# Optimization experiments

Hardware: AMD Instinct MI355X
Metric: run time of the kernel (lower is better)

## Reference

```python
import jax, jax.numpy as jnp
import numpy as np
import math

H = 5120        # hidden_size
NH = 32         # num heads
HD = H // NH    # head_dim = 160
B = 1
S = 2048
TRAIN_SEQLEN = 8192
BASE = 10000.0


def _rotary_cos_sin(seq_len):
    # Eval-mode RotaryEmbedding: seq_len clamped to training_seqlen, NTK alpha + mscale (logN) scaling.
    eff = max(seq_len, TRAIN_SEQLEN)
    scale = eff / TRAIN_SEQLEN
    mscale = 1.0 if scale <= 1.0 else 0.1 * math.log(scale) + 1.0
    ntk_alpha = max(2 ** math.ceil(math.log(eff / 4096, 2) + 1) - 1, 1)
    base = BASE * ntk_alpha ** (HD / (HD - 2))
    inv_freq = 1.0 / base ** (np.arange(0, HD, 2, dtype=np.float64) / HD)
    t = np.arange(eff, dtype=np.float64)
    freqs = np.outer(t, inv_freq)              # [eff, HD/2]
    emb = np.concatenate([freqs, freqs], axis=-1)  # [eff, HD]
    cos = (mscale * np.cos(emb))[:seq_len].astype(np.float32)
    sin = (mscale * np.sin(emb))[:seq_len].astype(np.float32)
    return jnp.asarray(cos), jnp.asarray(sin)


def _rotate_half(x):
    x1, x2 = x[..., : HD // 2], x[..., HD // 2 :]
    return jnp.concatenate([-x2, x1], axis=-1)


def setup_inputs() -> dict:
    key = jax.random.key(0)
    ks = jax.random.split(key, 6)
    hidden_states = jax.random.normal(ks[0], (B, S, H), jnp.float32)
    residual = jax.random.normal(ks[1], (B, S, H), jnp.float32)
    # boolean causal mask, True = masked (matches masked_fill semantics)
    attention_mask = jnp.triu(jnp.ones((S, S), dtype=bool), k=1)[None, None]
    Wq = jax.random.normal(ks[2], (H, H), jnp.float32) * 0.02      # query: Linear(h, h, bias=False)
    Wkv = jax.random.normal(ks[3], (2 * H, H), jnp.float32) * 0.02  # key_value: Linear(h, 2h, bias=False)
    Wd = jax.random.normal(ks[4], (H, H), jnp.float32) * 0.02       # dense: Linear(h, h) with bias
    bd = jnp.zeros((H,), jnp.float32)
    return {
        "hidden_states": hidden_states,
        "residual": residual,
        "attention_mask": attention_mask,
        "Wq": Wq,
        "Wkv": Wkv,
        "Wd": Wd,
        "bd": bd,
    }


def reference(hidden_states, residual, attention_mask, Wq, Wkv, Wd, bd):
    b, s, h = hidden_states.shape
    # QKV projections (torch Linear: y = x @ W.T)
    q = jnp.einsum('bsh,oh->bso', hidden_states, Wq).reshape(b, s, NH, HD)
    kv = jnp.einsum('bsh,oh->bso', hidden_states, Wkv).reshape(b, s, NH, 2 * HD)
    k, v = kv[..., :HD], kv[..., HD:]
    # rotary embedding with logN mscale folded into cos/sin
    cos, sin = _rotary_cos_sin(s)               # [s, HD]
    cos = cos[None, :, None, :]
    sin = sin[None, :, None, :]
    q = q * cos + _rotate_half(q) * sin
    k = k * cos + _rotate_half(k) * sin
    inv_norm = 1.0 / math.sqrt(HD)
    scores = jnp.einsum('bqnd,bknd->bnqk', q, k) * inv_norm   # [b, nh, s, s]
    scores = jnp.where(attention_mask, jnp.finfo(scores.dtype).min, scores)
    probs = jax.nn.softmax(scores, axis=-1)
    # attention_dropout p=0.0 -> identity
    ctx = jnp.einsum('bnqk,bknd->bqnd', probs, v).reshape(b, s, h)
    out = ctx @ Wd.T + bd
    # dropout_add with hidden_dropout=0.0 (eval) -> residual + out
    return residual + out
```

## Files before the change

kernel.cpp:

```cpp
#include <hip/hip_runtime.h>
#include <cmath>

typedef unsigned short u16;
typedef unsigned int   u32;

using bf16x8 = __attribute__((ext_vector_type(8))) short;
using f32x4  = __attribute__((ext_vector_type(4))) float;

#define S_LEN 2048
#define NHEAD 32
#define HDIM  160
#define HID   5120
#define NQKV  15360

__device__ __forceinline__ f32x4 mfma16(bf16x8 a, bf16x8 b, f32x4 c) {
  return __builtin_amdgcn_mfma_f32_16x16x32_bf16(a, b, c, 0, 0, 0);
}

__device__ __forceinline__ u16 f2bf(float f) {
  u32 u = __builtin_bit_cast(u32, f);
  u += 0x7FFFu + ((u >> 16) & 1u);
  return (u16)(u >> 16);
}
__device__ __forceinline__ float bf2f(u16 h) {
  u32 u = ((u32)h) << 16;
  return __builtin_bit_cast(float, u);
}

__device__ __forceinline__ void gload16(const void* g, void* l) {
  __builtin_amdgcn_global_load_lds((const __attribute__((address_space(1))) void*)g,
                                   (__attribute__((address_space(3))) void*)l, 16, 0, 0);
}

__global__ void cvt_bf16_kernel(const float* __restrict__ in, u16* __restrict__ out, int n8) {
  int i = blockIdx.x * 256 + threadIdx.x;
  if (i >= n8) return;
  const float4* p = (const float4*)in + (size_t)i * 2;
  float4 a = p[0], b = p[1];
  uint4 o;
  o.x = (u32)f2bf(a.x) | ((u32)f2bf(a.y) << 16);
  o.y = (u32)f2bf(a.z) | ((u32)f2bf(a.w) << 16);
  o.z = (u32)f2bf(b.x) | ((u32)f2bf(b.y) << 16);
  o.w = (u32)f2bf(b.z) | ((u32)f2bf(b.w) << 16);
  ((uint4*)out)[i] = o;
}

__global__ void rope_table_kernel(float2* __restrict__ tab) {
  __shared__ double invf_s[80];
  int tid = threadIdx.x;
  if (tid < 80) {
    double base = 10000.0 * pow(3.0, 160.0 / 158.0);
    invf_s[tid] = pow(base, -((double)(2 * tid)) / 160.0);
  }
  __syncthreads();
  for (int i = blockIdx.x * 256 + tid; i < S_LEN * 80; i += gridDim.x * 256) {
    int s = i / 80, j = i % 80;
    double ang = fmod((double)s * invf_s[j], 6.283185307179586476925287);
    float a = (float)ang;
    tab[i] = make_float2(cosf(a), sinf(a));
  }
}

__global__ void rope_apply_kernel(const u16* __restrict__ src, const float2* __restrict__ tab,
                                  u16* __restrict__ dst, int headStride, int rowStride) {
  int i = blockIdx.x * 256 + threadIdx.x;
  if (i >= S_LEN * NHEAD * 80) return;
  int dp = i % 80; int sh = i / 80; int h = sh % NHEAD; int s = sh / NHEAD;
  int d = 2 * dp;
  const u16* row = src + (size_t)s * rowStride + h * headStride;
  u32 q01 = *(const u32*)&row[d];
  u32 p01 = *(const u32*)&row[d < 80 ? d + 80 : d - 80];
  int j = (d < 80) ? d : d - 80;
  float2 cs0 = tab[s * 80 + j];
  float2 cs1 = tab[s * 80 + j + 1];
  float q0 = bf2f((u16)(q01 & 0xffff)), q1 = bf2f((u16)(q01 >> 16));
  float p0 = bf2f((u16)(p01 & 0xffff)), p1 = bf2f((u16)(p01 >> 16));
  float sgn = (d < 80) ? -1.f : 1.f;
  float o0 = q0 * cs0.x + sgn * p0 * cs0.y;
  float o1 = q1 * cs1.x + sgn * p1 * cs1.y;
  u32 o = (u32)f2bf(o0) | ((u32)f2bf(o1) << 16);
  *(u32*)&dst[((size_t)h * S_LEN + s) * HDIM + d] = o;
}

__global__ void vtrans_kernel(const u16* __restrict__ src, u16* __restrict__ Vt, int rowStride) {
  __shared__ u16 T[HDIM][72];
  int h = blockIdx.y; int s0 = blockIdx.x * 64; int tid = threadIdx.x;
  for (int i = tid; i < 64 * 80; i += 256) {
    int s = i / 80, dp = i % 80;
    u32 v = *(const u32*)&src[(size_t)(s0 + s) * rowStride + h * 320 + 2 * dp];
    T[2 * dp][s]     = (u16)(v & 0xffff);
    T[2 * dp + 1][s] = (u16)(v >> 16);
  }
  __syncthreads();
  for (int i = tid; i < HDIM * 32; i += 256) {
    int d = i / 32, sp = i % 32;
    u32 v = (u32)T[d][2 * sp] | ((u32)T[d][2 * sp + 1] << 16);
    *(u32*)&Vt[((size_t)h * HDIM + d) * S_LEN + s0 + 2 * sp] = v;
  }
}

template<int EPI>
__global__ __launch_bounds__(512, 2) void gemm256(
    const u16* __restrict__ A, const u16* __restrict__ Bm, void* __restrict__ Cout,
    int M, int N, int K, const float* __restrict__ bias, const float* __restrict__ resid)
{
  __shared__ u16 As[2][2][8192];
  __shared__ u16 Bs[2][2][8192];
  int tid = threadIdx.x;
  int w = tid >> 6, l = tid & 63, l15 = l & 15, l4 = l >> 4;
  int wr = w >> 2, wc = w & 3;

  int nbx = gridDim.x;
  int nwg = nbx * gridDim.y;
  int lin = blockIdx.y * nbx + blockIdx.x;
  int cpx = nwg >> 3;
  int swz = (lin & 7) * cpx + (lin >> 3);
  int bm = (swz / nbx) * 256, bn = (swz % nbx) * 256;

  int srow = tid >> 2;
  int scol = ((tid & 3) * 8) ^ ((srow & 8) ? 16 : 0);
  const u16* gA0 = A  + (size_t)(bm +       srow) * K + scol;
  const u16* gA1 = A  + (size_t)(bm + 128 + srow) * K + scol;
  const u16* gB0 = Bm + (size_t)(bn +       srow) * K + scol;
  const u16* gB1 = Bm + (size_t)(bn + 128 + srow) * K + scol;
  int dstoff = w * 512;

  f32x4 acc[8][4];
#pragma unroll
  for (int i = 0; i < 8; i++)
#pragma unroll
    for (int j = 0; j < 4; j++) acc[i][j] = f32x4{0.f, 0.f, 0.f, 0.f};

  int cA = (l4 * 8) ^ ((l15 & 8) ? 16 : 0);
  const int NT = K >> 6;

  auto STAGE = [&](int kt, int p) {
    int k0 = kt << 6;
    gload16(gA0 + k0,      &As[p][0][dstoff]);
    gload16(gA0 + k0 + 32, &As[p][0][4096 + dstoff]);
    gload16(gA1 + k0,      &As[p][1][dstoff]);
    gload16(gA1 + k0 + 32, &As[p][1][4096 + dstoff]);
    gload16(gB0 + k0,      &Bs[p][0][dstoff]);
    gload16(gB0 + k0 + 32, &Bs[p][0][4096 + dstoff]);
    gload16(gB1 + k0,      &Bs[p][1][dstoff]);
    gload16(gB1 + k0 + 32, &Bs[p][1][4096 + dstoff]);
  };

  STAGE(0, 0);
  for (int kt = 0; kt < NT; ++kt) {
    int p = kt & 1;
    if (kt + 1 < NT) {
      STAGE(kt + 1, p ^ 1);
      asm volatile("s_waitcnt vmcnt(8)" ::: "memory");
    } else {
      asm volatile("s_waitcnt vmcnt(0)" ::: "memory");
    }
    __builtin_amdgcn_s_barrier();

    const u16* Ah = &As[p][wr][0];
    const u16* Bh = &Bs[p][wc >> 1][0];
    int bcol = (wc & 1) * 64;
#pragma unroll
    for (int kk = 0; kk < 2; ++kk) {
      bf16x8 aF[8], bF[4];
#pragma unroll
      for (int mi = 0; mi < 8; ++mi)
        aF[mi] = *(const bf16x8*)&Ah[kk * 4096 + (mi * 16 + l15) * 32 + cA];
#pragma unroll
      for (int ni = 0; ni < 4; ++ni)
        bF[ni] = *(const bf16x8*)&Bh[kk * 4096 + (bcol + ni * 16 + l15) * 32 + cA];
      __builtin_amdgcn_s_setprio(1);
#pragma unroll
      for (int mi = 0; mi < 8; ++mi)
#pragma unroll
        for (int ni = 0; ni < 4; ++ni)
          acc[mi][ni] = mfma16(aF[mi], bF[ni], acc[mi][ni]);
      __builtin_amdgcn_s_setprio(0);
    }
    __builtin_amdgcn_s_barrier();
  }

#pragma unroll
  for (int mi = 0; mi < 8; ++mi)
#pragma unroll
    for (int ni = 0; ni < 4; ++ni) {
      int row0 = bm + wr * 128 + mi * 16 + l4 * 4;
      int col  = bn + wc * 64 + ni * 16 + l15;
      if (EPI == 0) {
        u16* C = (u16*)Cout;
#pragma unroll
        for (int r = 0; r < 4; r++) C[(size_t)(row0 + r) * N + col] = f2bf(acc[mi][ni][r]);
      } else {
        float* C = (float*)Cout;
        float b = bias[col];
#pragma unroll
        for (int r = 0; r < 4; r++) {
          size_t idx = (size_t)(row0 + r) * N + col;
          C[idx] = acc[mi][ni][r] + b + resid[idx];
        }
      }
    }
}

template<int EPI>
__global__ __launch_bounds__(256, 2) void gemm_bt(
    const u16* __restrict__ A, const u16* __restrict__ Bm, void* __restrict__ Cout,
    int M, int N, int K, const float* __restrict__ bias, const float* __restrict__ resid)
{
  int tid = threadIdx.x;
  int wv = tid >> 6, l = tid & 63, l15 = l & 15, l4 = l >> 4;
  int nbx = gridDim.x;
  int nwg = nbx * gridDim.y;
  int lin = blockIdx.y * nbx + blockIdx.x;
  int cpx = nwg >> 3;
  int swz = (lin & 7) * cpx + (lin >> 3);
  int bm = (swz / nbx) * 128, bn = (swz % nbx) * 128;

  __shared__ u16 As[128 * 32], Bs[128 * 32];
  f32x4 acc[4][4];
#pragma unroll
  for (int i = 0; i < 4; i++)
#pragma unroll
    for (int j = 0; j < 4; j++) acc[i][j] = f32x4{0.f, 0.f, 0.f, 0.f};

  int wm = (wv >> 1) * 64, wn = (wv & 1) * 64;
  const u16* gA = A + (size_t)(bm + (tid >> 2)) * K + (tid & 3) * 8;
  const u16* gB = Bm + (size_t)(bn + (tid >> 2)) * K + (tid & 3) * 8;
  u16* ldsA = As + wv * 16 * 32;
  u16* ldsB = Bs + wv * 16 * 32;

  for (int k0 = 0; k0 < K; k0 += 32) {
    __syncthreads();
    gload16(gA + k0, ldsA);
    gload16(gA + (size_t)64 * K + k0, ldsA + 64 * 32);
    gload16(gB + k0, ldsB);
    gload16(gB + (size_t)64 * K + k0, ldsB + 64 * 32);
    __syncthreads();
    bf16x8 af[4], bfr[4];
#pragma unroll
    for (int i = 0; i < 4; i++) af[i] = *(const bf16x8*)&As[(wm + i * 16 + l15) * 32 + l4 * 8];
#pragma unroll
    for (int i = 0; i < 4; i++) bfr[i] = *(const bf16x8*)&Bs[(wn + i * 16 + l15) * 32 + l4 * 8];
#pragma unroll
    for (int mi = 0; mi < 4; mi++)
#pragma unroll
      for (int ni = 0; ni < 4; ni++) acc[mi][ni] = mfma16(af[mi], bfr[ni], acc[mi][ni]);
  }

#pragma unroll
  for (int mi = 0; mi < 4; mi++)
#pragma unroll
    for (int ni = 0; ni < 4; ni++) {
      int row0 = bm + wm + mi * 16 + l4 * 4;
      int col  = bn + wn + ni * 16 + l15;
      if (EPI == 0) {
        u16* C = (u16*)Cout;
#pragma unroll
        for (int r = 0; r < 4; r++) C[(size_t)(row0 + r) * N + col] = f2bf(acc[mi][ni][r]);
      } else {
        float* C = (float*)Cout;
        float b = bias[col];
#pragma unroll
        for (int r = 0; r < 4; r++) {
          size_t idx = (size_t)(row0 + r) * N + col;
          C[idx] = acc[mi][ni][r] + b + resid[idx];
        }
      }
    }
}

__global__ __launch_bounds__(512, 4) void attn_kernel(
    const u16* __restrict__ Qr, const u16* __restrict__ Kr,
    const u16* __restrict__ Vt, u16* __restrict__ ctx)
{
  int lin = blockIdx.x;
  int h  = lin & 31;
  int qx = (lin < 256) ? (15 - (lin >> 5)) : ((lin - 256) >> 5);
  int q0 = qx * 128;
  int tid = threadIdx.x;
  int w = tid >> 6, l = tid & 63, l15 = l & 15, l4 = l >> 4;
  int qb = q0 + w * 16;

  __shared__ u16 Ks[64][164];
  __shared__ u16 Vs[160][68];
  __shared__ u16 Plds[8][16][68];

  const u16* Qh = Qr + (size_t)h * S_LEN * HDIM;
  const u16* Kh = Kr + (size_t)h * S_LEN * HDIM;
  const u16* Vh = Vt + (size_t)h * HDIM * S_LEN;

  bf16x8 aQ[5];
#pragma unroll
  for (int kc = 0; kc < 5; kc++)
    aQ[kc] = *(const bf16x8*)&Qh[(size_t)(qb + l15) * HDIM + kc * 32 + l4 * 8];

  f32x4 accO[10];
#pragma unroll
  for (int dt = 0; dt < 10; dt++) accO[dt] = f32x4{0.f, 0.f, 0.f, 0.f};
  float mrun[4], lrun[4];
#pragma unroll
  for (int r = 0; r < 4; r++) { mrun[r] = -1e30f; lrun[r] = 0.f; }

  const float c2 = 0.07905694150420949f * 1.44269504088896f;
  int Tend = 2 * qx + 2;

  {
    uint4 rg[5];
#pragma unroll
    for (int i = 0; i < 5; i++) {
      int u = tid + 512 * i;
      if (u < 1280) { int row = u / 20, c = u % 20;
        rg[i] = *(const uint4*)&Kh[(size_t)row * HDIM + c * 8]; }
      else { int v = u - 1280; int row = v >> 3, c = v & 7;
        rg[i] = *(const uint4*)&Vh[(size_t)row * S_LEN + c * 8]; }
    }
#pragma unroll
    for (int i = 0; i < 5; i++) {
      int u = tid + 512 * i;
      if (u < 1280) { int row = u / 20, c = u % 20; *(uint4*)&Ks[row][c * 8] = rg[i]; }
      else { int v = u - 1280; int row = v >> 3, c = v & 7; *(uint4*)&Vs[row][c * 8] = rg[i]; }
    }
  }
  __syncthreads();

  for (int t = 0; t < Tend; ++t) {
    int k0 = t * 64;
    bool more = (t + 1 < Tend);
    uint4 rg[5];
    if (more) {
      int k1 = k0 + 64;
#pragma unroll
      for (int i = 0; i < 5; i++) {
        int u = tid + 512 * i;
        if (u < 1280) { int row = u / 20, c = u % 20;
          rg[i] = *(const uint4*)&Kh[(size_t)(k1 + row) * HDIM + c * 8]; }
        else { int v = u - 1280; int row = v >> 3, c = v & 7;
          rg[i] = *(const uint4*)&Vh[(size_t)row * S_LEN + k1 + c * 8]; }
      }
    }

    if (k0 <= qb + 15) {
      f32x4 s_[4];
#pragma unroll
      for (int nt = 0; nt < 4; nt++) s_[nt] = f32x4{0.f, 0.f, 0.f, 0.f};

#pragma unroll
      for (int kc = 0; kc < 5; kc++) {
        bf16x8 bK[4];
#pragma unroll
        for (int nt = 0; nt < 4; nt++)
          bK[nt] = *(const bf16x8*)&Ks[nt * 16 + l15][kc * 32 + l4 * 8];
        __builtin_amdgcn_s_setprio(1);
#pragma unroll
        for (int nt = 0; nt < 4; nt++) s_[nt] = mfma16(aQ[kc], bK[nt], s_[nt]);
        __builtin_amdgcn_s_setprio(0);
      }

      if (k0 + 63 > qb) {
#pragma unroll
        for (int nt = 0; nt < 4; nt++)
#pragma unroll
          for (int r = 0; r < 4; r++) {
            int kk = k0 + nt * 16 + l15;
            int qq = qb + l4 * 4 + r;
            if (kk > qq) s_[nt][r] = -1e30f;
          }
      }

      float sf[4];
#pragma unroll
      for (int r = 0; r < 4; r++) {
        float v = fmaxf(fmaxf(s_[0][r], s_[1][r]), fmaxf(s_[2][r], s_[3][r]));
#pragma unroll
        for (int m = 1; m <= 8; m <<= 1) v = fmaxf(v, __shfl_xor(v, m));
        float mnew = fmaxf(mrun[r], v);
        sf[r] = exp2f((mrun[r] - mnew) * c2);
        mrun[r] = mnew;
      }
      float rsum[4] = {0.f, 0.f, 0.f, 0.f};
#pragma unroll
      for (int nt = 0; nt < 4; nt++)
#pragma unroll
        for (int r = 0; r < 4; r++) {
          float p = exp2f((s_[nt][r] - mrun[r]) * c2);
          s_[nt][r] = p;
          rsum[r] += p;
        }
#pragma unroll
      for (int r = 0; r < 4; r++) {
        float v = rsum[r];
#pragma unroll
        for (int m = 1; m <= 8; m <<= 1) v += __shfl_xor(v, m);
        lrun[r] = lrun[r] * sf[r] + v;
      }
#pragma unroll
      for (int dt = 0; dt < 10; dt++)
#pragma unroll
        for (int r = 0; r < 4; r++) accO[dt][r] *= sf[r];
#pragma unroll
      for (int nt = 0; nt < 4; nt++)
#pragma unroll
        for (int r = 0; r < 4; r++)
          Plds[w][l4 * 4 + r][nt * 16 + l15] = f2bf(s_[nt][r]);

#pragma unroll
      for (int kc = 0; kc < 2; kc++) {
        bf16x8 aP = *(const bf16x8*)&Plds[w][l15][kc * 32 + l4 * 8];
        bf16x8 bV[10];
#pragma unroll
        for (int dt = 0; dt < 10; dt++)
          bV[dt] = *(const bf16x8*)&Vs[dt * 16 + l15][kc * 32 + l4 * 8];
        __builtin_amdgcn_s_setprio(1);
#pragma unroll
        for (int dt = 0; dt < 10; dt++)
          accO[dt] = mfma16(aP, bV[dt], accO[dt]);
        __builtin_amdgcn_s_setprio(0);
      }
    }

    __builtin_amdgcn_s_barrier();
    if (more) {
#pragma unroll
      for (int i = 0; i < 5; i++) {
        int u = tid + 512 * i;
        if (u < 1280) { int row = u / 20, c = u % 20; *(uint4*)&Ks[row][c * 8] = rg[i]; }
        else { int v = u - 1280; int row = v >> 3, c = v & 7; *(uint4*)&Vs[row][c * 8] = rg[i]; }
      }
      asm volatile("s_waitcnt lgkmcnt(0)" ::: "memory");
    }
    __builtin_amdgcn_s_barrier();
  }

  float inv[4];
#pragma unroll
  for (int r = 0; r < 4; r++) inv[r] = 1.0f / lrun[r];
#pragma unroll
  for (int dt = 0; dt < 10; dt++)
#pragma unroll
    for (int r = 0; r < 4; r++) {
      int q = qb + l4 * 4 + r;
      ctx[(size_t)q * HID + h * HDIM + dt * 16 + l15] = f2bf(accO[dt][r] * inv[r]);
    }
}

extern "C" void kernel_launch(void* const* d_in, const int* in_sizes, int n_in,
                              void* d_out, int out_size, void* d_ws, size_t ws_size,
                              hipStream_t stream) {
  const float* hs    = (const float*)d_in[0];
  const float* resid = (const float*)d_in[1];
  const float* Wq  = (const float*)d_in[3];
  const float* Wkv = (const float*)d_in[4];
  const float* Wd  = (const float*)d_in[5];
  const float* bd  = (const float*)d_in[6];
  float* out = (float*)d_out;

  char* ws = (char*)d_ws;
  const size_t SH = (size_t)S_LEN * HID;
  u16* Xb     = (u16*)(ws);                        size_t off = SH * 2;
  u16* Wqkvb  = (u16*)(ws + off);                  off += (size_t)3 * HID * HID * 2;
  u16* Wdb    = (u16*)(ws + off);                  off += (size_t)HID * HID * 2;
  u16* QKVraw = (u16*)(ws + off);                  off += (size_t)S_LEN * NQKV * 2;
  u16* Qr     = (u16*)(ws + off);                  off += SH * 2;
  u16* Kr     = (u16*)(ws + off);                  off += SH * 2;
  u16* Vt     = (u16*)(ws + off);                  off += SH * 2;
  u16* ctx    = (u16*)(ws + off);                  off += SH * 2;
  float2* tab = (float2*)(ws + off);               off += (size_t)S_LEN * 80 * 8;

  cvt_bf16_kernel<<<(int)(SH / 8 / 256), 256, 0, stream>>>(hs, Xb, (int)(SH / 8));
  cvt_bf16_kernel<<<HID * HID / 8 / 256, 256, 0, stream>>>(Wq, Wqkvb, HID * HID / 8);
  cvt_bf16_kernel<<<2 * HID * HID / 8 / 256, 256, 0, stream>>>(Wkv, Wqkvb + (size_t)HID * HID, 2 * HID * HID / 8);
  cvt_bf16_kernel<<<HID * HID / 8 / 256, 256, 0, stream>>>(Wd, Wdb, HID * HID / 8);

  rope_table_kernel<<<64, 256, 0, stream>>>(tab);

  gemm256<0><<<dim3(NQKV / 256, S_LEN / 256), 512, 0, stream>>>(
      Xb, Wqkvb, QKVraw, S_LEN, NQKV, HID, nullptr, nullptr);

  rope_apply_kernel<<<S_LEN * NHEAD * 80 / 256, 256, 0, stream>>>(QKVraw, tab, Qr, HDIM, NQKV);
  rope_apply_kernel<<<S_LEN * NHEAD * 80 / 256, 256, 0, stream>>>(QKVraw + HID, tab, Kr, 2 * HDIM, NQKV);
  vtrans_kernel<<<dim3(S_LEN / 64, NHEAD), 256, 0, stream>>>(QKVraw + HID + HDIM, Vt, NQKV);

  attn_kernel<<<512, 512, 0, stream>>>(Qr, Kr, Vt, ctx);

  gemm_bt<1><<<dim3(HID / 128, S_LEN / 128), 256, 0, stream>>>(
      ctx, Wdb, out, S_LEN, HID, HID, bd, resid);
}
```

Baseline: 1.008 ms.

## Split GEMM k-loop into four phases with staggered A/B prefetch

Restructures the bf16 MFMA GEMM main loop into four sub-phases, each covering one k-half and one half of the M rows. Each phase issues one slice of the global-to-LDS prefetch for later tiles (A or B, one k-half), so loads spread across the iteration instead of arriving in one burst. The LDS buffers are reorganised by k-half, and loads run up to two tiles ahead with adjusted vmcnt waits. Register pressure for A fragments drops from 8 to 4 per phase. The cost is many more workgroup barriers per iteration and more complex wait accounting, which could stall the waves.

```diff
diff --git a/kernel.cpp b/kernel.cpp
--- a/kernel.cpp
+++ b/kernel.cpp
@@ -119,11 +119,9 @@
 
   int srow = tid >> 2;
   int scol = ((tid & 3) * 8) ^ ((srow & 8) ? 16 : 0);
-  const u16* gA0 = A  + (size_t)(bm +       srow) * K + scol;
-  const u16* gA1 = A  + (size_t)(bm + 128 + srow) * K + scol;
-  const u16* gB0 = Bm + (size_t)(bn +       srow) * K + scol;
-  const u16* gB1 = Bm + (size_t)(bn + 128 + srow) * K + scol;
-  int dstoff = w * 512;
+  const u16* gAr = A  + (size_t)(bm + srow) * K + scol;
+  const u16* gBr = Bm + (size_t)(bn + srow) * K + scol;
+  int w512 = w * 512;
 
   f32x4 acc[8][4];
 #pragma unroll
@@ -133,50 +131,87 @@
 
   int cA = (l4 * 8) ^ ((l15 & 8) ? 16 : 0);
   const int NT = K >> 6;
-
-  auto STAGE = [&](int kt, int p) {
-    int k0 = kt << 6;
-    gload16(gA0 + k0,      &As[p][0][dstoff]);
-    gload16(gA0 + k0 + 32, &As[p][0][4096 + dstoff]);
-    gload16(gA1 + k0,      &As[p][1][dstoff]);
-    gload16(gA1 + k0 + 32, &As[p][1][4096 + dstoff]);
-    gload16(gB0 + k0,      &Bs[p][0][dstoff]);
-    gload16(gB0 + k0 + 32, &Bs[p][0][4096 + dstoff]);
-    gload16(gB1 + k0,      &Bs[p][1][dstoff]);
-    gload16(gB1 + k0 + 32, &Bs[p][1][4096 + dstoff]);
-  };
-
-  STAGE(0, 0);
+  int arow = wr * 128;
+  int brow = (wc >> 1) * 128 + (wc & 1) * 64;
+
+  auto STA = [&](int kt, int kk) { int p = kt & 1, ko = (kt << 6) + (kk << 5);
+    gload16(gAr + ko, &As[p][kk][w512]);
+    gload16(gAr + (size_t)128 * K + ko, &As[p][kk][4096 + w512]); };
+  auto STB = [&](int kt, int kk) { int p = kt & 1, ko = (kt << 6) + (kk << 5);
+    gload16(gBr + ko, &Bs[p][kk][w512]);
+    gload16(gBr + (size_t)128 * K + ko, &Bs[p][kk][4096 + w512]); };
+
+  STB(0, 0); STA(0, 0); STB(0, 1); STA(0, 1);
+  if (NT > 1) { STB(1, 0); STA(1, 0); STB(1, 1); }
+  asm volatile("s_waitcnt vmcnt(6)" ::: "memory");
+  __builtin_amdgcn_s_barrier();
+
   for (int kt = 0; kt < NT; ++kt) {
     int p = kt & 1;
-    if (kt + 1 < NT) {
-      STAGE(kt + 1, p ^ 1);
-      asm volatile("s_waitcnt vmcnt(8)" ::: "memory");
-    } else {
-      asm volatile("s_waitcnt vmcnt(0)" ::: "memory");
-    }
-    __builtin_amdgcn_s_barrier();
-
-    const u16* Ah = &As[p][wr][0];
-    const u16* Bh = &Bs[p][wc >> 1][0];
-    int bcol = (wc & 1) * 64;
-#pragma unroll
-    for (int kk = 0; kk < 2; ++kk) {
-      bf16x8 aF[8], bF[4];
-#pragma unroll
-      for (int mi = 0; mi < 8; ++mi)
-        aF[mi] = *(const bf16x8*)&Ah[kk * 4096 + (mi * 16 + l15) * 32 + cA];
+    bf16x8 aF[4], bF0[4], bF1[4];
+
+    if (kt + 1 < NT) STA(kt + 1, 1);
+#pragma unroll
+    for (int mi = 0; mi < 4; ++mi)
+      aF[mi] = *(const bf16x8*)&As[p][0][(arow + mi * 16 + l15) * 32 + cA];
+#pragma unroll
+    for (int ni = 0; ni < 4; ++ni)
+      bF0[ni] = *(const bf16x8*)&Bs[p][0][(brow + ni * 16 + l15) * 32 + cA];
+    __builtin_amdgcn_s_barrier();
+    __builtin_amdgcn_s_setprio(1);
+#pragma unroll
+    for (int mi = 0; mi < 4; ++mi)
 #pragma unroll
       for (int ni = 0; ni < 4; ++ni)
-        bF[ni] = *(const bf16x8*)&Bh[kk * 4096 + (bcol + ni * 16 + l15) * 32 + cA];
-      __builtin_amdgcn_s_setprio(1);
-#pragma unroll
-      for (int mi = 0; mi < 8; ++mi)
-#pragma unroll
-        for (int ni = 0; ni < 4; ++ni)
-          acc[mi][ni] = mfma16(aF[mi], bF[ni], acc[mi][ni]);
-      __builtin_amdgcn_s_setprio(0);
-    }
+        acc[mi][ni] = mfma16(aF[mi], bF0[ni], acc[mi][ni]);
+    __builtin_amdgcn_s_setprio(0);
+    __builtin_amdgcn_s_barrier();
+
+    if (kt + 2 < NT) STB(kt + 2, 0);
+#pragma unroll
+    for (int mi = 0; mi < 4; ++mi)
+      aF[mi] = *(const bf16x8*)&As[p][0][(arow + 64 + mi * 16 + l15) * 32 + cA];
+    __builtin_amdgcn_s_barrier();
+    __builtin_amdgcn_s_setprio(1);
+#pragma unroll
+    for (int mi = 0; mi < 4; ++mi)
+#pragma unroll
+      for (int ni = 0; ni < 4; ++ni)
+        acc[4 + mi][ni] = mfma16(aF[mi], bF0[ni], acc[4 + mi][ni]);
+    __builtin_amdgcn_s_setprio(0);
+    __builtin_amdgcn_s_barrier();
+
+    if (kt + 2 < NT) STA(kt + 2, 0);
+#pragma unroll
+    for (int mi = 0; mi < 4; ++mi)
+      aF[mi] = *(const bf16x8*)&As[p][1][(arow + mi * 16 + l15) * 32 + cA];
+#pragma unroll
+    for (int ni = 0; ni < 4; ++ni)
+      bF1[ni] = *(const bf16x8*)&Bs[p][1][(brow + ni * 16 + l15) * 32 + cA];
+    __builtin_amdgcn_s_barrier();
+    __builtin_amdgcn_s_setprio(1);
+#pragma unroll
+    for (int mi = 0; mi < 4; ++mi)
+#pragma unroll
+      for (int ni = 0; ni < 4; ++ni)
+        acc[mi][ni] = mfma16(aF[mi], bF1[ni], acc[mi][ni]);
+    __builtin_amdgcn_s_setprio(0);
+    __builtin_amdgcn_s_barrier();
+
+    if (kt + 2 < NT) STB(kt + 2, 1);
+#pragma unroll
+    for (int mi = 0; mi < 4; ++mi)
+      aF[mi] = *(const bf16x8*)&As[p][1][(arow + 64 + mi * 16 + l15) * 32 + cA];
+    __builtin_amdgcn_s_barrier();
+    __builtin_amdgcn_s_setprio(1);
+#pragma unroll
+    for (int mi = 0; mi < 4; ++mi)
+#pragma unroll
+      for (int ni = 0; ni < 4; ++ni)
+        acc[4 + mi][ni] = mfma16(aF[mi], bF1[ni], acc[4 + mi][ni]);
+    __builtin_amdgcn_s_setprio(0);
+    if (kt + 2 < NT)      asm volatile("s_waitcnt vmcnt(6)" ::: "memory");
+    else if (kt + 1 < NT) asm volatile("s_waitcnt vmcnt(0)" ::: "memory");
     __builtin_amdgcn_s_barrier();
   }
 
```

Result: faster. 980.8 us (-2.7%).
